# Kernel optimization log

Measured on AMD Instinct MI355X. Metric: run time of the kernel, lower is better.

Reference implementation:

```python
import jax, jax.numpy as jnp
import numpy as np

T, A, B_IMG, Z, READ_N, WRITE_N, ENC, DEC, BATCH = 16, 64, 64, 128, 8, 8, 512, 512, 512
EPS = 1e-8


def setup_inputs() -> dict:
    key = jax.random.key(0)
    ks = jax.random.split(key, 16)
    s = 0.05
    n = lambda k, shape: jax.random.normal(k, shape, jnp.float32) * s
    return {
        "x": jax.random.uniform(ks[0], (BATCH, B_IMG * A), jnp.float32),
        "eps": jax.random.normal(ks[1], (T, BATCH, Z), jnp.float32),
        "enc_Wih": n(ks[2], (4 * ENC, 2 * READ_N * READ_N + DEC)),
        "enc_Whh": n(ks[3], (4 * ENC, ENC)),
        "enc_b": jnp.zeros((4 * ENC,), jnp.float32),
        "mu_W": n(ks[4], (Z, ENC)),
        "mu_b": jnp.zeros((Z,), jnp.float32),
        "sig_W": n(ks[5], (Z, ENC)),
        "sig_b": jnp.zeros((Z,), jnp.float32),
        "dec_Wih": n(ks[6], (4 * DEC, Z)),
        "dec_Whh": n(ks[7], (4 * DEC, DEC)),
        "dec_b": jnp.zeros((4 * DEC,), jnp.float32),
        "write_W": n(ks[8], (WRITE_N * WRITE_N, DEC)),
        "write_b": jnp.zeros((WRITE_N * WRITE_N,), jnp.float32),
        "attn_W": n(ks[9], (5, DEC)),
        "attn_b": jnp.zeros((5,), jnp.float32),
    }


def _lstm(x, h, c, Wih, Whh, b):
    g = x @ Wih.T + h @ Whh.T + b  # [bs, 4H]
    i, f, gg, o = jnp.split(g, 4, axis=1)
    c2 = jax.nn.sigmoid(f) * c + jax.nn.sigmoid(i) * jnp.tanh(gg)
    return jax.nn.sigmoid(o) * jnp.tanh(c2), c2


def _filterbank(gx, gy, sigma2, delta, N):
    # gx, gy, sigma2, delta: [bs, 1]
    grid = jnp.arange(N, dtype=jnp.float32)[None, :]  # [1, N]
    mu_x = gx + (grid - 0.5 * N - 0.5) * delta  # [bs, N]
    mu_y = gy + (grid - 0.5 * N - 0.5) * delta
    a = jnp.arange(A, dtype=jnp.float32)
    b = jnp.arange(B_IMG, dtype=jnp.float32)
    s2 = sigma2[:, :, None]  # [bs,1,1]
    Fx = jnp.exp(-((a[None, None, :] - mu_x[:, :, None]) ** 2) / (2 * s2))  # [bs,N,A]
    Fx = Fx / (Fx.sum(2, keepdims=True) + EPS)
    Fy = jnp.exp(-((b[None, None, :] - mu_y[:, :, None]) ** 2) / (2 * s2))  # [bs,N,B]
    Fy = Fy / (Fy.sum(2, keepdims=True) + EPS)
    return Fx, Fy


def _attn_window(h_dec, N, attn_W, attn_b):
    p = h_dec @ attn_W.T + attn_b  # [bs,5]
    gx_, gy_, log_s2, log_d, log_g = jnp.split(p, 5, axis=1)
    gx = (A + 1) * 0.5 * (gx_ + 1)
    gy = (B_IMG + 1) * 0.5 * (gy_ + 1)
    delta = (max(A, B_IMG) - 1) * jnp.exp(log_d) / (N - 1)
    Fx, Fy = _filterbank(gx, gy, jnp.exp(log_s2), delta, N)
    return Fx, Fy, jnp.exp(log_g)  # gamma: [bs,1]


def reference(x, eps, enc_Wih, enc_Whh, enc_b, mu_W, mu_b, sig_W, sig_b,
              dec_Wih, dec_Whh, dec_b, write_W, write_b, attn_W, attn_b):
    bs = x.shape[0]
    img = x.reshape(bs, B_IMG, A)

    def step(carry, e):
        h_enc, c_enc, h_dec, c_dec, canvas = carry
        x_hat = x - jax.nn.sigmoid(canvas)
        # --- read with attention ---
        Fx, Fy, gamma = _attn_window(h_dec, READ_N, attn_W, attn_b)
        def glimpse(im):  # Fy @ im @ Fx^T -> [bs, N, N]
            g = jnp.einsum('bnh,bhw,bmw->bnm', Fy, im, Fx)
            return g.reshape(bs, READ_N * READ_N) * gamma
        r = jnp.concatenate([glimpse(img), glimpse(x_hat.reshape(bs, B_IMG, A))], axis=1)
        # --- encoder LSTM ---
        h_enc, c_enc = _lstm(jnp.concatenate([r, h_dec], 1), h_enc, c_enc, enc_Wih, enc_Whh, enc_b)
        # --- latent sample ---
        mu = h_enc @ mu_W.T + mu_b
        log_sigma = h_enc @ sig_W.T + sig_b
        z = mu + e * jnp.exp(log_sigma)
        # --- decoder LSTM ---
        h_dec, c_dec = _lstm(z, h_dec, c_dec, dec_Wih, dec_Whh, dec_b)
        # --- write with attention ---
        w = (h_dec @ write_W.T + write_b).reshape(bs, WRITE_N, WRITE_N)
        Fx2, Fy2, gamma2 = _attn_window(h_dec, WRITE_N, attn_W, attn_b)
        wr = jnp.einsum('bnh,bnm,bma->bha', Fy2, w, Fx2).reshape(bs, B_IMG * A) / gamma2
        canvas = canvas + wr
        return (h_enc, c_enc, h_dec, c_dec, canvas), canvas

    z32 = jnp.zeros((bs, ENC), jnp.float32)
    init = (z32, z32, jnp.zeros((bs, DEC), jnp.float32), jnp.zeros((bs, DEC), jnp.float32),
            jnp.zeros((bs, B_IMG * A), jnp.float32))
    _, cs = jax.lax.scan(step, init, eps)
    return cs  # [T, bs, B*A]
```

## Files before the change

kernel.cpp:

```cpp
#include <hip/hip_runtime.h>

#define LDF 68
#define EPSF 1e-8f
#define MFMA(A,B,C) __builtin_amdgcn_mfma_f32_16x16x32_bf16((A),(B),(C),0,0,0)

typedef __attribute__((ext_vector_type(8))) short bf16x8;
typedef __attribute__((ext_vector_type(4))) float f32x4;

__device__ __forceinline__ float sigf(float x){ return 1.0f/(1.0f + __expf(-x)); }

__device__ __forceinline__ unsigned short f2bf(float f){
  unsigned u = __float_as_uint(f);
  u += 0x7FFFu + ((u >> 16) & 1u);
  return (unsigned short)(u >> 16);
}
__device__ __forceinline__ float bf2f(unsigned short s){
  return __uint_as_float((unsigned)s << 16);
}

__device__ __forceinline__ size_t pk(int b, int col, int KB){
  return ((((size_t)((b>>4)*KB + (col>>5)))*64) + (size_t)((b&15) + (((col>>3)&3)<<4)))*8 + (col&7);
}

__device__ __forceinline__ void gload_lds16(const void* g, void* l){
  __builtin_amdgcn_global_load_lds(
      (const __attribute__((address_space(1))) void*)g,
      (__attribute__((address_space(3))) void*)l, 16, 0, 0);
}

__global__ void reorder_gates(const float* __restrict__ src, float* __restrict__ dst,
                              int H, int K, int total){
  int idx = blockIdx.x*256 + threadIdx.x;
  if (idx >= total) return;
  int row = idx / K;
  int col = idx - row*K;
  int j = row >> 2, g = row & 3;
  dst[idx] = src[(size_t)(g*H + j)*K + col];
}

__global__ void pack_w_mfma(const float* __restrict__ Wih, const float* __restrict__ Whh,
                            int K_ih, int K_tot,
                            unsigned short* __restrict__ dhi, unsigned short* __restrict__ dlo,
                            int total8){
  int idx = blockIdx.x*256 + threadIdx.x;
  if (idx >= total8) return;
  int lane = idx & 63;
  int rest = idx >> 6;
  int KB = K_tot >> 5;
  int kb = rest % KB;
  int fm = rest / KB;
  int rr = fm*16 + (lane & 15);
  int orow = (rr & 3)*512 + (rr >> 2);
  int k0 = kb*32 + (lane >> 4)*8;
  union { unsigned short s[8]; uint4 u; } vh, vl;
  #pragma unroll
  for (int i = 0; i < 8; i++){
    int k = k0 + i;
    float f = (k < K_ih) ? Wih[(size_t)orow*K_ih + k]
                         : Whh[(size_t)orow*512 + (k - K_ih)];
    unsigned short hi = f2bf(f);
    vh.s[i] = hi;
    vl.s[i] = f2bf(f - bf2f(hi));
  }
  *(uint4*)(dhi + (size_t)idx*8) = vh.u;
  *(uint4*)(dlo + (size_t)idx*8) = vl.u;
}

__global__ void pack_wz_mfma(const float* __restrict__ muW, const float* __restrict__ sigW,
                             unsigned short* __restrict__ dhi, unsigned short* __restrict__ dlo){
  int idx = blockIdx.x*256 + threadIdx.x;
  if (idx >= 16384) return;
  int lane = idx & 63, rest = idx >> 6;
  int kb = rest & 15, fmf = rest >> 4;
  int row = fmf*16 + (lane & 15);
  const float* src = (row < 128) ? (muW + (size_t)row*512) : (sigW + (size_t)(row-128)*512);
  int k0 = kb*32 + (lane >> 4)*8;
  union { unsigned short s[8]; uint4 u; } vh, vl;
  #pragma unroll
  for (int i = 0; i < 8; i++){
    float f = src[k0 + i];
    unsigned short hi = f2bf(f);
    vh.s[i] = hi;
    vl.s[i] = f2bf(f - bf2f(hi));
  }
  *(uint4*)(dhi + (size_t)idx*8) = vh.u;
  *(uint4*)(dlo + (size_t)idx*8) = vl.u;
}

__global__ void transpose_ww(const float* __restrict__ W, float* __restrict__ dst){
  int idx = blockIdx.x*256 + threadIdx.x;
  if (idx >= 512*64) return;
  int k = idx >> 6, n = idx & 63;
  dst[idx] = W[n*512 + k];
}

__global__ void zero_f(float* p, int n){
  int idx = blockIdx.x*256 + threadIdx.x;
  if (idx < n) p[idx] = 0.f;
}

__device__ void attn_window(const float* __restrict__ h,
                            const float* __restrict__ attn_W,
                            const float* __restrict__ attn_b,
                            float* Fx, float* Fy, float* pl)
{
  int tid = threadIdx.x;
  int lane = tid & 63, wid = tid >> 6;
  for (int q = wid; q < 5; q += 4){
    float s = 0.f;
    for (int k = lane; k < 512; k += 64) s += h[k]*attn_W[q*512 + k];
    for (int m = 32; m; m >>= 1) s += __shfl_xor(s, m);
    if (lane == 0) pl[q] = s + attn_b[q];
  }
  __syncthreads();
  float gx    = 32.5f*(pl[0] + 1.f);
  float gy    = 32.5f*(pl[1] + 1.f);
  float s2    = __expf(pl[2]);
  float delta = 9.f*__expf(pl[3]);
  float inv2  = 1.f/(2.f*s2);
  int n = tid >> 5, a = tid & 31;
  float mux = gx + ((float)n - 4.5f)*delta;
  float muy = gy + ((float)n - 4.5f)*delta;
  float dx0 = (float)a      - mux, dx1 = (float)(a+32) - mux;
  float dy0 = (float)a      - muy, dy1 = (float)(a+32) - muy;
  float e0 = __expf(-dx0*dx0*inv2), e1 = __expf(-dx1*dx1*inv2);
  float f0 = __expf(-dy0*dy0*inv2), f1 = __expf(-dy1*dy1*inv2);
  float sx = e0 + e1, sy = f0 + f1;
  for (int m = 16; m; m >>= 1){ sx += __shfl_xor(sx, m); sy += __shfl_xor(sy, m); }
  float rx = 1.f/(sx + EPSF), ry = 1.f/(sy + EPSF);
  Fx[n*LDF + a]      = e0*rx;  Fx[n*LDF + a + 32] = e1*rx;
  Fy[n*LDF + a]      = f0*ry;  Fy[n*LDF + a + 32] = f1*ry;
  __syncthreads();
}

template<int KB>
__global__ __launch_bounds__(512) void mfma_gemm_lstm(
    const bf16x8* __restrict__ Wh, const bf16x8* __restrict__ Wl,
    const unsigned short* __restrict__ act, int actPlane,
    const float4* __restrict__ bias4, const float* __restrict__ c_in,
    float* __restrict__ h_f32, float* __restrict__ c_out,
    unsigned short* __restrict__ out0, int KB0, int off0, int plane0,
    unsigned short* __restrict__ out1, int KB1, int off1, int plane1)
{
  __shared__ __align__(16) unsigned char lds[2][8192];
  const int tid = threadIdx.x, lane = tid & 63, w = tid >> 6;
  const int mt = blockIdx.x & 31, nt = blockIdx.x >> 5;
  const int fm = w & 3, fn0 = (w >> 2) << 1;

  const bf16x8* whp = Wh + ((size_t)(mt*4+fm)*KB)*64 + lane;
  const bf16x8* wlp = Wl + ((size_t)(mt*4+fm)*KB)*64 + lane;

  const char* ast = (const char*)act + (size_t)(w & 1)*((size_t)actPlane*2)
                  + ((size_t)(nt*4 + (w >> 1))*KB)*1024 + (size_t)lane*16;
  char* myl0 = (char*)&lds[0][w*1024];
  char* myl1 = (char*)&lds[1][w*1024];

  const int j0 = (mt*4+fm)*4 + (lane >> 4);
  float4 bb = bias4[j0];
  f32x4 acc0 = {bb.x, bb.y, bb.z, bb.w};
  f32x4 acc1 = acc0;

  gload_lds16(ast, myl0);
  asm volatile("s_waitcnt vmcnt(0)");
  __syncthreads();

  const unsigned char* rb0 = &lds[0][fn0*2048];
  const unsigned char* rb1 = &lds[1][fn0*2048];

  bf16x8 whv = whp[0];
  bf16x8 wlv = wlp[0];

  for (int kb = 0; kb < KB; kb++){
    int cur = kb & 1;
    if (kb + 1 < KB) gload_lds16(ast + (size_t)(kb+1)*1024, cur ? myl0 : myl1);
    bf16x8 whn = whv, wln = wlv;
    if (kb + 1 < KB){ whn = whp[(kb+1)*64]; wln = wlp[(kb+1)*64]; }
    const unsigned char* rb = cur ? rb1 : rb0;
    bf16x8 a0h = *(const bf16x8*)(rb +        (size_t)lane*16);
    bf16x8 a0l = *(const bf16x8*)(rb + 1024 + (size_t)lane*16);
    bf16x8 a1h = *(const bf16x8*)(rb + 2048 + (size_t)lane*16);
    bf16x8 a1l = *(const bf16x8*)(rb + 3072 + (size_t)lane*16);
    acc0 = MFMA(whv, a0h, acc0);
    acc1 = MFMA(whv, a1h, acc1);
    acc0 = MFMA(wlv, a0h, acc0);
    acc1 = MFMA(wlv, a1h, acc1);
    acc0 = MFMA(whv, a0l, acc0);
    acc1 = MFMA(whv, a1l, acc1);
    __syncthreads();
    whv = whn; wlv = wln;
  }

  const int bb0 = nt*64 + fn0*16 + (lane & 15);
  #pragma unroll
  for (int n = 0; n < 2; n++){
    f32x4 g = n ? acc1 : acc0;
    int b = bb0 + n*16;
    float ig = sigf(g[0]);
    float fg = sigf(g[1]);
    float gg = tanhf(g[2]);
    float og = sigf(g[3]);
    float c2 = fg * c_in[(size_t)b*512 + j0] + ig * gg;
    float h  = og * tanhf(c2);
    c_out[(size_t)b*512 + j0] = c2;
    if (h_f32) h_f32[(size_t)b*512 + j0] = h;
    unsigned short hh = f2bf(h);
    unsigned short hl = f2bf(h - bf2f(hh));
    size_t o0 = pk(b, off0 + j0, KB0);
    out0[o0] = hh; out0[o0 + plane0] = hl;
    if (out1){
      size_t o1 = pk(b, off1 + j0, KB1);
      out1[o1] = hh; out1[o1 + plane1] = hl;
    }
  }
}

__global__ __launch_bounds__(64) void zgemm_kernel(
    const bf16x8* __restrict__ Wzh, const bf16x8* __restrict__ Wzl,
    const unsigned short* __restrict__ az, int planeZ,
    const float* __restrict__ mu_b, const float* __restrict__ sig_b,
    const float* __restrict__ eps_t,
    unsigned short* __restrict__ actD, int planeD)
{
  const int fmb = blockIdx.x & 7, cg = blockIdx.x >> 3;
  const int lane = threadIdx.x;
  const bf16x8* wmh = Wzh + (size_t)(fmb    *16)*64 + lane;
  const bf16x8* wml = Wzl + (size_t)(fmb    *16)*64 + lane;
  const bf16x8* wsh = Wzh + (size_t)((fmb+8)*16)*64 + lane;
  const bf16x8* wsl = Wzl + (size_t)((fmb+8)*16)*64 + lane;
  const unsigned short* ab = az + (size_t)cg*8192 + (size_t)lane*8;

  const int r0 = fmb*16 + (lane >> 4)*4;
  float4 bm = *(const float4*)&mu_b[r0];
  float4 bs = *(const float4*)&sig_b[r0];
  f32x4 am = {bm.x, bm.y, bm.z, bm.w};
  f32x4 as = {bs.x, bs.y, bs.z, bs.w};

  #pragma unroll
  for (int kb = 0; kb < 16; kb++){
    bf16x8 ah = *(const bf16x8*)(ab + (size_t)kb*512);
    bf16x8 al = *(const bf16x8*)(ab + planeZ + (size_t)kb*512);
    bf16x8 h0 = wmh[kb*64], l0 = wml[kb*64];
    bf16x8 h1 = wsh[kb*64], l1 = wsl[kb*64];
    am = MFMA(h0, ah, am); am = MFMA(l0, ah, am); am = MFMA(h0, al, am);
    as = MFMA(h1, ah, as); as = MFMA(l1, ah, as); as = MFMA(h1, al, as);
  }

  const int b = cg*16 + (lane & 15);
  float4 ev = *(const float4*)&eps_t[(size_t)b*128 + r0];
  float e[4] = {ev.x, ev.y, ev.z, ev.w};
  union { unsigned short s[4]; uint2 u; } zh, zl;
  #pragma unroll
  for (int i = 0; i < 4; i++){
    float z = am[i] + e[i]*__expf(as[i]);
    unsigned short hi = f2bf(z);
    zh.s[i] = hi;
    zl.s[i] = f2bf(z - bf2f(hi));
  }
  size_t o = pk(b, r0, 20);
  *(uint2*)(actD + o) = zh.u;
  *(uint2*)(actD + planeD + o) = zl.u;
}

__global__ __launch_bounds__(256) void wg_kernel(
    const float* __restrict__ h_dec,
    const float* __restrict__ WwT, const float* __restrict__ write_b,
    const float* __restrict__ attn_W, const float* __restrict__ attn_b,
    const float* __restrict__ canvas_prev, float* __restrict__ canvas_out,
    const float* __restrict__ x,
    unsigned short* __restrict__ rout, int planeE)
{
  __shared__ float hs[512];
  __shared__ float Fx[8*LDF], Fy[8*LDF], pl[8];
  __shared__ float cs[64*LDF];
  __shared__ float img_s[64*LDF];
  __shared__ float P[2][8*LDF];
  __shared__ float ps[4][64], w_s[64];
  __shared__ float tmp[64*8];
  const int b = blockIdx.x, tid = threadIdx.x;

  for (int i = tid; i < 128; i += 256)
    ((float4*)hs)[i] = ((const float4*)(h_dec + (size_t)b*512))[i];
  if (rout){
    const float4* x4 = (const float4*)(x + (size_t)b*4096);
    for (int i = tid; i < 1024; i += 256){
      int row = i >> 4, cb = (i & 15)*4;
      *(float4*)&img_s[row*LDF + cb] = x4[i];
    }
  }
  __syncthreads();
  attn_window(hs, attn_W, attn_b, Fx, Fy, pl);
  float gamma = __expf(pl[4]);

  if (canvas_out){
    {
      int j = tid & 63, part = tid >> 6;
      float s = 0.f;
      int kb = part*128;
      for (int k = 0; k < 128; k++) s += hs[kb + k] * WwT[(kb + k)*64 + j];
      ps[part][j] = s;
    }
    __syncthreads();
    if (tid < 64)
      w_s[tid] = write_b[tid] + ps[0][tid] + ps[1][tid] + ps[2][tid] + ps[3][tid];
    __syncthreads();
    float inv_g = __expf(-pl[4]);
    #pragma unroll
    for (int e = 0; e < 2; e++){
      int gi = e*256 + tid;
      int m = gi & 7, hh = gi >> 3;
      float s = 0.f;
      #pragma unroll
      for (int nn = 0; nn < 8; nn++) s += Fy[nn*LDF + hh] * w_s[nn*8 + m];
      tmp[hh*8 + m] = s;
    }
    __syncthreads();
    for (int e = 0; e < 16; e++){
      int idx = e*256 + tid;
      int hh = idx >> 6, a = idx & 63;
      float s = 0.f;
      #pragma unroll
      for (int m = 0; m < 8; m++) s += tmp[hh*8 + m] * Fx[m*LDF + a];
      float prev = canvas_prev ? canvas_prev[(size_t)b*4096 + idx] : 0.f;
      float cv = prev + s*inv_g;
      canvas_out[(size_t)b*4096 + idx] = cv;
      cs[hh*LDF + a] = cv;
    }
  } else {
    for (int e = 0; e < 16; e++){
      int idx = e*256 + tid;
      cs[(idx >> 6)*LDF + (idx & 63)] = 0.f;
    }
  }
  if (!rout) return;
  __syncthreads();
  for (int e = 0; e < 16; e++){
    int idx = e*256 + tid;
    int hh = idx >> 6, a = idx & 63;
    cs[hh*LDF + a] = sigf(cs[hh*LDF + a]);
  }
  __syncthreads();
  #pragma unroll
  for (int e = 0; e < 4; e++){
    int gi = e*256 + tid;
    int d = gi >> 9, rem = gi & 511;
    int m = rem & 7, hh = rem >> 3;
    const float* S = d ? cs : img_s;
    float s = 0.f;
    #pragma unroll
    for (int w4 = 0; w4 < 64; w4 += 4){
      float4 iv = *(const float4*)&S[hh*LDF + w4];
      float4 fv = *(const float4*)&Fx[m*LDF + w4];
      s += iv.x*fv.x + iv.y*fv.y + iv.z*fv.z + iv.w*fv.w;
    }
    P[d][m*LDF + hh] = s;
  }
  __syncthreads();
  if (tid < 128){
    int d = tid >> 6, l = tid & 63;
    int n = l >> 3, m = l & 7;
    float s = 0.f;
    #pragma unroll
    for (int h4 = 0; h4 < 64; h4 += 4){
      float4 fv = *(const float4*)&Fy[n*LDF + h4];
      float4 pv = *(const float4*)&P[d][m*LDF + h4];
      s += fv.x*pv.x + fv.y*pv.y + fv.z*pv.z + fv.w*pv.w;
    }
    tmp[d*64 + l] = s;
  }
  __syncthreads();
  if (tid < 64){
    float g1 = tmp[tid]*gamma;
    float g2 = (tmp[tid] - tmp[64 + tid])*gamma;
    unsigned short h1 = f2bf(g1), l1 = f2bf(g1 - bf2f(h1));
    unsigned short h2 = f2bf(g2), l2 = f2bf(g2 - bf2f(h2));
    size_t o1 = pk(b, tid, 36);
    size_t o2 = pk(b, 64 + tid, 36);
    rout[o1] = h1; rout[o1 + planeE] = l1;
    rout[o2] = h2; rout[o2 + planeE] = l2;
  }
}

extern "C" void kernel_launch(void* const* d_in, const int* in_sizes, int n_in,
                              void* d_out, int out_size, void* d_ws, size_t ws_size,
                              hipStream_t stream)
{
  (void)in_sizes; (void)n_in; (void)out_size; (void)ws_size;
  const float* x       = (const float*)d_in[0];
  const float* eps     = (const float*)d_in[1];
  const float* encWih  = (const float*)d_in[2];
  const float* encWhh  = (const float*)d_in[3];
  const float* enc_b   = (const float*)d_in[4];
  const float* muW     = (const float*)d_in[5];
  const float* mu_b    = (const float*)d_in[6];
  const float* sigW    = (const float*)d_in[7];
  const float* sig_b   = (const float*)d_in[8];
  const float* decWih  = (const float*)d_in[9];
  const float* decWhh  = (const float*)d_in[10];
  const float* dec_b   = (const float*)d_in[11];
  const float* writeW  = (const float*)d_in[12];
  const float* write_b = (const float*)d_in[13];
  const float* attnW   = (const float*)d_in[14];
  const float* attn_b  = (const float*)d_in[15];
  float* out = (float*)d_out;

  char* p = (char*)d_ws;
  auto alloc = [&](size_t bytes){ char* r = p; p += (bytes + 255) & ~(size_t)255; return r; };

  const int KE = 1152, KD = 640;
  const int PE = 512*KE, PD = 512*KD, PZ = 512*512;
  const int T8E = 128*36*64, T8D = 128*20*64;

  unsigned short* WpEh = (unsigned short*)alloc((size_t)T8E*16);
  unsigned short* WpEl = (unsigned short*)alloc((size_t)T8E*16);
  unsigned short* WpDh = (unsigned short*)alloc((size_t)T8D*16);
  unsigned short* WpDl = (unsigned short*)alloc((size_t)T8D*16);
  unsigned short* Wzh  = (unsigned short*)alloc(16384*16);
  unsigned short* Wzl  = (unsigned short*)alloc(16384*16);
  float* bE  = (float*)alloc(2048*4);
  float* bD  = (float*)alloc(2048*4);
  float* WwT = (float*)alloc(512*64*4);
  char* z0 = p;
  unsigned short* actE0 = (unsigned short*)alloc((size_t)2*PE*2);
  unsigned short* actD0 = (unsigned short*)alloc((size_t)2*PD*2);
  float* hDf = (float*)alloc(512*512*4);
  float* cE0 = (float*)alloc(512*512*4);
  float* cD0 = (float*)alloc(512*512*4);
  size_t zbytes = (size_t)(p - z0);
  unsigned short* actE1 = (unsigned short*)alloc((size_t)2*PE*2);
  unsigned short* actD1 = (unsigned short*)alloc((size_t)2*PD*2);
  unsigned short* AZ    = (unsigned short*)alloc((size_t)2*PZ*2);
  float* cE1 = (float*)alloc(512*512*4);
  float* cD1 = (float*)alloc(512*512*4);

  unsigned short* actE[2] = { actE0, actE1 };
  unsigned short* actD[2] = { actD0, actD1 };
  float* cEf[2] = { cE0, cE1 };
  float* cDf[2] = { cD0, cD1 };

  int tot;
  tot = T8E;   pack_w_mfma<<<(tot+255)/256,256,0,stream>>>(encWih, encWhh, 640, KE, WpEh, WpEl, tot);
  tot = T8D;   pack_w_mfma<<<(tot+255)/256,256,0,stream>>>(decWih, decWhh, 128, KD, WpDh, WpDl, tot);
  pack_wz_mfma<<<64,256,0,stream>>>(muW, sigW, Wzh, Wzl);
  tot = 2048;  reorder_gates<<<(tot+255)/256,256,0,stream>>>(enc_b, bE, 512, 1, tot);
  tot = 2048;  reorder_gates<<<(tot+255)/256,256,0,stream>>>(dec_b, bD, 512, 1, tot);
  tot = 512*64; transpose_ww<<<(tot+255)/256,256,0,stream>>>(writeW, WwT);
  tot = (int)(zbytes/4); zero_f<<<(tot+255)/256,256,0,stream>>>((float*)z0, tot);

  wg_kernel<<<512,256,0,stream>>>(hDf, WwT, write_b, attnW, attn_b,
                                  nullptr, nullptr, x, actE[0], PE);

  for (int t = 0; t < 16; t++){
    int cur = t & 1, nxt = cur ^ 1;

    mfma_gemm_lstm<36><<<256,512,0,stream>>>(
        (const bf16x8*)WpEh, (const bf16x8*)WpEl, actE[cur], PE,
        (const float4*)bE, cEf[cur], nullptr, cEf[nxt],
        AZ, 16, 0, PZ,
        actE[nxt], 36, 640, PE);

    zgemm_kernel<<<256,64,0,stream>>>(
        (const bf16x8*)Wzh, (const bf16x8*)Wzl, AZ, PZ,
        mu_b, sig_b, eps + (size_t)t*65536, actD[cur], PD);

    mfma_gemm_lstm<20><<<256,512,0,stream>>>(
        (const bf16x8*)WpDh, (const bf16x8*)WpDl, actD[cur], PD,
        (const float4*)bD, cDf[cur], hDf, cDf[nxt],
        actE[nxt], 36, 128, PE,
        actD[nxt], 20, 128, PD);

    wg_kernel<<<512,256,0,stream>>>(hDf, WwT, write_b, attnW, attn_b,
                                    t ? (out + (size_t)(t-1)*2097152) : nullptr,
                                    out + (size_t)t*2097152, x,
                                    (t < 15) ? actE[nxt] : nullptr, PE);
  }
}
```

Before: 1.092 ms.

## Triple-buffer LDS activations in the LSTM MFMA GEMM with prefetch distance two

Replaces the double-buffered activation and weight prefetch in the LSTM GEMM loop with a three-stage ring that prefetches two K-blocks ahead. Each iteration now needs a single barrier plus an explicit partial vmcnt wait, instead of a full sync after the MFMAs. The loop is also fully unrolled so buffer indices become constants. The aim is to hide more global-load latency and cut barrier stalls, at the cost of 8 KB more LDS per block. The fixed vmcnt(3) wait assumes three loads are always in flight, which may not hold in the last iterations where no new loads are issued.

```diff
diff --git a/kernel.cpp b/kernel.cpp
--- a/kernel.cpp
+++ b/kernel.cpp
@@ -142,7 +142,7 @@
     unsigned short* __restrict__ out0, int KB0, int off0, int plane0,
     unsigned short* __restrict__ out1, int KB1, int off1, int plane1)
 {
-  __shared__ __align__(16) unsigned char lds[2][8192];
+  __shared__ __align__(16) unsigned char lds[3][8192];
   const int tid = threadIdx.x, lane = tid & 63, w = tid >> 6;
   const int mt = blockIdx.x & 31, nt = blockIdx.x >> 5;
   const int fm = w & 3, fn0 = (w >> 2) << 1;
@@ -152,42 +152,46 @@
 
   const char* ast = (const char*)act + (size_t)(w & 1)*((size_t)actPlane*2)
                   + ((size_t)(nt*4 + (w >> 1))*KB)*1024 + (size_t)lane*16;
-  char* myl0 = (char*)&lds[0][w*1024];
-  char* myl1 = (char*)&lds[1][w*1024];
 
   const int j0 = (mt*4+fm)*4 + (lane >> 4);
   float4 bb = bias4[j0];
   f32x4 acc0 = {bb.x, bb.y, bb.z, bb.w};
   f32x4 acc1 = acc0;
 
-  gload_lds16(ast, myl0);
-  asm volatile("s_waitcnt vmcnt(0)");
-  __syncthreads();
-
-  const unsigned char* rb0 = &lds[0][fn0*2048];
-  const unsigned char* rb1 = &lds[1][fn0*2048];
-
-  bf16x8 whv = whp[0];
-  bf16x8 wlv = wlp[0];
-
+  gload_lds16(ast, (char*)&lds[0][w*1024]);
+  bf16x8 whA = whp[0], wlA = wlp[0];
+  __builtin_amdgcn_sched_barrier(0);
+  asm volatile("" ::: "memory");
+  gload_lds16(ast + 1024, (char*)&lds[1][w*1024]);
+  bf16x8 whB = whp[64], wlB = wlp[64];
+  __builtin_amdgcn_sched_barrier(0);
+  asm volatile("" ::: "memory");
+
+  const size_t rdoff = (size_t)fn0*2048 + (size_t)lane*16;
+
+  #pragma unroll
   for (int kb = 0; kb < KB; kb++){
-    int cur = kb & 1;
-    if (kb + 1 < KB) gload_lds16(ast + (size_t)(kb+1)*1024, cur ? myl0 : myl1);
-    bf16x8 whn = whv, wln = wlv;
-    if (kb + 1 < KB){ whn = whp[(kb+1)*64]; wln = wlp[(kb+1)*64]; }
-    const unsigned char* rb = cur ? rb1 : rb0;
-    bf16x8 a0h = *(const bf16x8*)(rb +        (size_t)lane*16);
-    bf16x8 a0l = *(const bf16x8*)(rb + 1024 + (size_t)lane*16);
-    bf16x8 a1h = *(const bf16x8*)(rb + 2048 + (size_t)lane*16);
-    bf16x8 a1l = *(const bf16x8*)(rb + 3072 + (size_t)lane*16);
-    acc0 = MFMA(whv, a0h, acc0);
-    acc1 = MFMA(whv, a1h, acc1);
-    acc0 = MFMA(wlv, a0h, acc0);
-    acc1 = MFMA(wlv, a1h, acc1);
-    acc0 = MFMA(whv, a0l, acc0);
-    acc1 = MFMA(whv, a1l, acc1);
-    __syncthreads();
-    whv = whn; wlv = wln;
+    asm volatile("s_waitcnt vmcnt(3)" ::: "memory");
+    __builtin_amdgcn_s_barrier();
+    asm volatile("" ::: "memory");
+    __builtin_amdgcn_sched_barrier(0);
+    bf16x8 whC = whA, wlC = wlA;
+    if (kb + 2 < KB){
+      gload_lds16(ast + (size_t)(kb+2)*1024, (char*)&lds[(kb+2)%3][w*1024]);
+      whC = whp[(kb+2)*64]; wlC = wlp[(kb+2)*64];
+    }
+    const unsigned char* rb = &lds[kb%3][0] + rdoff;
+    bf16x8 a0h = *(const bf16x8*)(rb);
+    bf16x8 a0l = *(const bf16x8*)(rb + 1024);
+    bf16x8 a1h = *(const bf16x8*)(rb + 2048);
+    bf16x8 a1l = *(const bf16x8*)(rb + 3072);
+    acc0 = MFMA(whA, a0h, acc0);
+    acc1 = MFMA(whA, a1h, acc1);
+    acc0 = MFMA(wlA, a0h, acc0);
+    acc1 = MFMA(wlA, a1h, acc1);
+    acc0 = MFMA(whA, a0l, acc0);
+    acc1 = MFMA(whA, a1l, acc1);
+    whA = whB; wlA = wlB; whB = whC; wlB = wlC;
   }
 
   const int bb0 = nt*64 + fn0*16 + (lane & 15);
```

New measurement: 933.4 us. 1.17x faster.
